# Kernel optimization log

Hardware: AMD Instinct MI355X
Metric: run time of the kernel (lower is better)

The kernel has to match this reference:

```python
import jax, jax.numpy as jnp
import numpy as np

LN_EPS = 1e-5

def layer_norm(x, g, b):
    m = x.mean(-1, keepdims=True)
    v = ((x - m) ** 2).mean(-1, keepdims=True)
    return (x - m) / jnp.sqrt(v + LN_EPS) * g + b

def gat_conv(x, src, dst, W, att_src, att_dst, bias, heads, out_ch, concat):
    # PyG GATConv (eval mode, self-loops already included in src/dst).
    N = x.shape[0]
    h = (x @ W).reshape(N, heads, out_ch)                 # [N,H,C]
    a_src = (h * att_src).sum(-1)                          # [N,H]
    a_dst = (h * att_dst).sum(-1)                          # [N,H]
    e = jax.nn.leaky_relu(a_src[src] + a_dst[dst], 0.2)   # [E,H]
    emax = jax.ops.segment_max(e, dst, num_segments=N)    # [N,H]
    ee = jnp.exp(e - emax[dst])
    denom = jax.ops.segment_sum(ee, dst, num_segments=N)  # [N,H]
    alpha = ee / (denom[dst] + 1e-16)                      # [E,H]
    out = jax.ops.segment_sum(alpha[:, :, None] * h[src], dst, num_segments=N)  # [N,H,C]
    out = out.reshape(N, heads * out_ch) if concat else out.mean(axis=1)
    return out + bias

def setup_inputs() -> dict:
    key = jax.random.key(0)
    ks = jax.random.split(key, 32)
    N, G, E = 50000, 405, 300000
    RH, GH, H = 256, 256, 4
    def w(k, shape, fan_in):
        return jax.random.normal(k, shape, dtype=jnp.float32) * (1.0 / np.sqrt(fan_in))
    d = {}
    d["x"] = jax.random.normal(ks[0], (N, G), dtype=jnp.float32)
    d["edge_index"] = jax.random.randint(ks[1], (2, E), 0, N, dtype=jnp.int64)
    # JointEncoder
    d["enc_w1"] = w(ks[2], (G, RH), G); d["enc_b1"] = jnp.zeros(RH)
    d["ln1_g"] = jnp.ones(RH); d["ln1_b"] = jnp.zeros(RH)
    d["enc_w2"] = w(ks[3], (RH, RH), RH); d["enc_b2"] = jnp.zeros(RH)
    d["ln2_g"] = jnp.ones(RH); d["ln2_b"] = jnp.zeros(RH)
    d["w1"] = w(ks[4], (RH, H * GH), RH)
    d["att_src1"] = w(ks[5], (H, GH), GH); d["att_dst1"] = w(ks[6], (H, GH), GH)
    d["bias1"] = jnp.zeros(H * GH)
    d["res1_w"] = w(ks[7], (RH, H * GH), RH); d["res1_b"] = jnp.zeros(H * GH)
    d["w2"] = w(ks[8], (H * GH, 2 * 96), H * GH)
    d["att_src2"] = w(ks[9], (2, 96), 96); d["att_dst2"] = w(ks[10], (2, 96), 96)
    d["bias2"] = jnp.zeros(2 * 96)
    d["res2_w"] = w(ks[11], (H * GH, 2 * 96), H * GH); d["res2_b"] = jnp.zeros(2 * 96)
    d["w3"] = w(ks[12], (192, 128), 192)
    d["att_src3"] = w(ks[13], (1, 128), 128); d["att_dst3"] = w(ks[14], (1, 128), 128)
    d["bias3"] = jnp.zeros(128)
    d["res3_w"] = w(ks[15], (192, 128), 192); d["res3_b"] = jnp.zeros(128)
    # MLP head
    d["mlp_w1"] = w(ks[16], (128, 64), 128); d["mlp_b1"] = jnp.zeros(64)
    d["mlp_w2"] = w(ks[17], (64, 2), 64); d["mlp_b2"] = jnp.zeros(2)
    return d

def reference(x, edge_index, enc_w1, enc_b1, ln1_g, ln1_b, enc_w2, enc_b2, ln2_g, ln2_b,
              w1, att_src1, att_dst1, bias1, res1_w, res1_b,
              w2, att_src2, att_dst2, bias2, res2_w, res2_b,
              w3, att_src3, att_dst3, bias3, res3_w, res3_b,
              mlp_w1, mlp_b1, mlp_w2, mlp_b2):
    N = x.shape[0]
    loop = jnp.arange(N, dtype=edge_index.dtype)
    src = jnp.concatenate([edge_index[0], loop])
    dst = jnp.concatenate([edge_index[1], loop])
    # JointEncoder (eval: dropout is identity)
    h = jax.nn.relu(layer_norm(x @ enc_w1 + enc_b1, ln1_g, ln1_b))
    h = jax.nn.relu(layer_norm(h @ enc_w2 + enc_b2, ln2_g, ln2_b))
    # Block 1
    idn = h
    h = jax.nn.elu(gat_conv(h, src, dst, w1, att_src1, att_dst1, bias1, 4, 256, True))
    h = h + (idn @ res1_w + res1_b)
    # Block 2
    idn = h
    h = jax.nn.elu(gat_conv(h, src, dst, w2, att_src2, att_dst2, bias2, 2, 96, True))
    h = h + (idn @ res2_w + res2_b)
    # Block 3
    idn = h
    h = jax.nn.elu(gat_conv(h, src, dst, w3, att_src3, att_dst3, bias3, 1, 128, False))
    h = h + (idn @ res3_w + res3_b)
    # MLP head
    out = jax.nn.relu(h @ mlp_w1 + mlp_b1) @ mlp_w2 + mlp_b2
    return out
```

## Files before the change

### kernel.cpp

```cpp
#include <hip/hip_runtime.h>
#include <cstddef>

#define LN_EPS 1e-5f

typedef __bf16 bf16x8 __attribute__((ext_vector_type(8)));
typedef float  f32x4  __attribute__((ext_vector_type(4)));

typedef __attribute__((address_space(3))) unsigned int lds_u32;
typedef __attribute__((address_space(1))) unsigned int glb_u32;

__device__ __forceinline__ void gl2lds16(const void* g, void* l) {
    __builtin_amdgcn_global_load_lds((const glb_u32*)g, (lds_u32*)l, 16, 0, 0);
}

__device__ __forceinline__ float b2f(ushort h) {
    return __uint_as_float(((unsigned)h) << 16);
}
__device__ __forceinline__ ushort f2b(float f) {
    unsigned u = __float_as_uint(f);
    return (ushort)((u + 0x7fffu + ((u >> 16) & 1u)) >> 16);
}
__device__ __forceinline__ unsigned pack2(float lo, float hi) {
    return (unsigned)f2b(lo) | ((unsigned)f2b(hi) << 16);
}
__device__ __forceinline__ uint2 pack4(const f32x4 v) {
    return make_uint2(pack2(v[0], v[1]), pack2(v[2], v[3]));
}

__device__ __forceinline__ void xcd_map(int& bx, int& by) {
    int NX = gridDim.x, MBr = gridDim.y;
    int L = blockIdx.y * NX + blockIdx.x;
    int G = NX * 8;
    int g = L / G;
    if (g * 8 + 8 <= MBr) {
        int r = L - g * G;
        by = g * 8 + (r & 7);
        bx = r >> 3;
    } else {
        by = L / NX;
        bx = L - by * NX;
    }
}

__device__ __forceinline__ float wave_allreduce_max(float v) {
    #pragma unroll
    for (int off = 32; off > 0; off >>= 1) v = fmaxf(v, __shfl_xor(v, off, 64));
    return v;
}
__device__ __forceinline__ float wave_allreduce_sum(float v) {
    #pragma unroll
    for (int off = 32; off > 0; off >>= 1) v += __shfl_xor(v, off, 64);
    return v;
}

__device__ __forceinline__ void stage32(const ushort* a0, const ushort* a1,
                                        const ushort* b0, const ushort* b1,
                                        ushort* __restrict__ As, ushort* __restrict__ Bs,
                                        int lb0, int lb1) {
    gl2lds16(a0, As + lb0);
    gl2lds16(a1, As + lb1);
    gl2lds16(b0, Bs + lb0);
    gl2lds16(b1, Bs + lb1);
}

__device__ __forceinline__ void mfma_loop32(const ushort* aA0, const ushort* aA1,
                                            const ushort* aB0, const ushort* aB1,
                                            ushort* __restrict__ As, ushort* __restrict__ Bs,
                                            int lb0, int lb1,
                                            int K, int wr, int wc, int cA, int l15,
                                            f32x4 acc[4][4]) {
    const int BUF = 128 * 32;
    const int nk = K >> 5;
    stage32(aA0, aA1, aB0, aB1, As, Bs, lb0, lb1);
    if (nk > 1) stage32(aA0 + 32, aA1 + 32, aB0 + 32, aB1 + 32,
                        As + BUF, Bs + BUF, lb0, lb1);
    int cur = 0;
    for (int t = 0; t < nk; t++) {
        if (t + 1 < nk) asm volatile("s_waitcnt vmcnt(4)" ::: "memory");
        else            asm volatile("s_waitcnt vmcnt(0)" ::: "memory");
        __builtin_amdgcn_s_barrier();
        __builtin_amdgcn_sched_barrier(0);
        int kn = (t + 2) * 32;
        if (kn < K) {
            int nb = cur + 2; if (nb >= 3) nb -= 3;
            stage32(aA0 + kn, aA1 + kn, aB0 + kn, aB1 + kn,
                    As + nb * BUF, Bs + nb * BUF, lb0, lb1);
        }
        const ushort* Ac = As + cur * BUF;
        const ushort* Bc = Bs + cur * BUF;
        bf16x8 af[4], bf[4];
        #pragma unroll
        for (int i = 0; i < 4; i++)
            af[i] = *reinterpret_cast<const bf16x8*>(&Ac[(wr + i * 16 + l15) * 32 + cA]);
        #pragma unroll
        for (int j = 0; j < 4; j++)
            bf[j] = *reinterpret_cast<const bf16x8*>(&Bc[(wc + j * 16 + l15) * 32 + cA]);
        #pragma unroll
        for (int i = 0; i < 4; i++)
            #pragma unroll
            for (int j = 0; j < 4; j++)
                acc[i][j] = __builtin_amdgcn_mfma_f32_16x16x32_bf16(bf[j], af[i], acc[i][j], 0, 0, 0);
        cur++; if (cur >= 3) cur -= 3;
    }
    __syncthreads();
}

template<int EPI>
__global__ __launch_bounds__(256) void bgemm(const ushort* __restrict__ A,
                                             const ushort* __restrict__ BT,
                                             const float* __restrict__ bias,
                                             void* __restrict__ out, int ldc,
                                             float* __restrict__ Rf,
                                             float* __restrict__ Sf, int Fs,
                                             int M, int Ncols, int K, int lda) {
    __shared__ ushort As[3][128 * 32];
    __shared__ ushort Bs[3][128 * 32];
    const int tid = threadIdx.x;
    int bx, by; xcd_map(bx, by);
    const int m0 = by * 128, n0 = bx * 128;
    const int w = tid >> 6, lane = tid & 63;
    const int wr = (w >> 1) * 64, wc = (w & 1) * 64;
    const int quad = lane >> 4, l15 = lane & 15;
    const int cA = (quad ^ ((l15 >> 1) & 3)) * 8;
    const int lb0 = w * 512, lb1 = lb0 + 2048;

    const int s0 = tid, s1 = tid + 256;
    const int r0 = s0 >> 2, g0 = ((s0 & 3) ^ ((s0 >> 3) & 3)) * 8;
    const int r1 = s1 >> 2, g1 = ((s1 & 3) ^ ((s1 >> 3) & 3)) * 8;
    int ga0 = m0 + r0; if (ga0 >= M) ga0 = M - 1;
    int ga1 = m0 + r1; if (ga1 >= M) ga1 = M - 1;
    const ushort* aA0 = A + (size_t)ga0 * lda + g0;
    const ushort* aA1 = A + (size_t)ga1 * lda + g1;
    const ushort* aB0 = BT + (size_t)(n0 + r0) * K + g0;
    const ushort* aB1 = BT + (size_t)(n0 + r1) * K + g1;

    f32x4 acc[4][4] = {};
    mfma_loop32(aA0, aA1, aB0, aB1, As[0], Bs[0], lb0, lb1,
                K, wr, wc, cA, l15, acc);

    if (EPI == 4) {
        if (wc == 0) {
            #pragma unroll
            for (int i = 0; i < 4; i++) {
                float o0 = 0.f, o1 = 0.f;
                #pragma unroll
                for (int j = 0; j < 4; j++) {
                    int colbase = j * 16 + quad * 4;
                    float4 bv = *reinterpret_cast<const float4*>(&bias[colbase]);
                    float bb[4] = { bv.x, bv.y, bv.z, bv.w };
                    #pragma unroll
                    for (int r = 0; r < 4; r++) {
                        float vv = fmaxf(acc[i][j][r] + bb[r], 0.f);
                        int c = colbase + r;
                        o0 += vv * Rf[2 * c];
                        o1 += vv * Rf[2 * c + 1];
                    }
                }
                o0 += __shfl_xor(o0, 16, 64); o0 += __shfl_xor(o0, 32, 64);
                o1 += __shfl_xor(o1, 16, 64); o1 += __shfl_xor(o1, 32, 64);
                int row = m0 + wr + i * 16 + l15;
                if (quad == 0 && row < M) {
                    ((float*)out)[(size_t)row * 2]     = o0 + Sf[0];
                    ((float*)out)[(size_t)row * 2 + 1] = o1 + Sf[1];
                }
            }
        }
        return;
    }

    const int twoH = Ncols - 2 * Fs;
    #pragma unroll
    for (int i = 0; i < 4; i++) {
        int row = m0 + wr + i * 16 + l15;
        if (row >= M) continue;
        #pragma unroll
        for (int j = 0; j < 4; j++) {
            int colbase = n0 + wc + j * 16 + quad * 4;
            if (EPI == 0) {
                f32x4 v = acc[i][j];
                if (bias) {
                    float4 bv = *reinterpret_cast<const float4*>(&bias[colbase]);
                    v[0] += bv.x; v[1] += bv.y; v[2] += bv.z; v[3] += bv.w;
                }
                *reinterpret_cast<f32x4*>(&((float*)out)[(size_t)row * ldc + colbase]) = v;
            } else if (EPI == 5) {
                if (colbase + 3 < Fs) {
                    *reinterpret_cast<uint2*>(&((ushort*)out)[(size_t)row * Fs + colbase]) = pack4(acc[i][j]);
                } else if (colbase >= Fs && colbase + 3 < 2 * Fs) {
                    *reinterpret_cast<f32x4*>(&Rf[(size_t)row * Fs + (colbase - Fs)]) = acc[i][j];
                } else {
                    #pragma unroll
                    for (int r = 0; r < 4; r++) {
                        int col = colbase + r;
                        if (col < 2 * Fs || col >= Ncols) continue;
                        Sf[(size_t)row * twoH + (col - 2 * Fs)] = acc[i][j][r];
                    }
                }
            }
        }
    }
}

__global__ __launch_bounds__(256) void bgemm_b1(const ushort* __restrict__ accb,
                                                const ushort* __restrict__ w1T,
                                                const ushort* __restrict__ h1b,
                                                const ushort* __restrict__ res1T,
                                                const float* __restrict__ bias1,
                                                const float* __restrict__ res1b,
                                                ushort* __restrict__ H2b, int M) {
    __shared__ ushort As[3][128 * 32];
    __shared__ ushort Bs[3][128 * 32];
    const int tid = threadIdx.x;
    int bx, by; xcd_map(bx, by);
    const int m0 = by * 128, n0 = bx * 128;
    const int h = n0 >> 8;
    const int w = tid >> 6, lane = tid & 63;
    const int wr = (w >> 1) * 64, wc = (w & 1) * 64;
    const int quad = lane >> 4, l15 = lane & 15;
    const int cA = (quad ^ ((l15 >> 1) & 3)) * 8;
    const int lb0 = w * 512, lb1 = lb0 + 2048;

    const int s0 = tid, s1 = tid + 256;
    const int r0 = s0 >> 2, g0 = ((s0 & 3) ^ ((s0 >> 3) & 3)) * 8;
    const int r1 = s1 >> 2, g1 = ((s1 & 3) ^ ((s1 >> 3) & 3)) * 8;
    int ga0 = m0 + r0; if (ga0 >= M) ga0 = M - 1;
    int ga1 = m0 + r1; if (ga1 >= M) ga1 = M - 1;

    f32x4 acc[4][4] = {};

    mfma_loop32(accb + (size_t)ga0 * 1024 + h * 256 + g0,
                accb + (size_t)ga1 * 1024 + h * 256 + g1,
                w1T + (size_t)(n0 + r0) * 256 + g0,
                w1T + (size_t)(n0 + r1) * 256 + g1,
                As[0], Bs[0], lb0, lb1, 256, wr, wc, cA, l15, acc);

    #pragma unroll
    for (int i = 0; i < 4; i++) {
        #pragma unroll
        for (int j = 0; j < 4; j++) {
            int colbase = n0 + wc + j * 16 + quad * 4;
            float4 bv = *reinterpret_cast<const float4*>(&bias1[colbase]);
            float4 rv = *reinterpret_cast<const float4*>(&res1b[colbase]);
            float bb[4] = { bv.x, bv.y, bv.z, bv.w };
            float rr[4] = { rv.x, rv.y, rv.z, rv.w };
            #pragma unroll
            for (int r = 0; r < 4; r++) {
                float t = acc[i][j][r] + bb[r];
                t = t > 0.f ? t : (__expf(t) - 1.f);
                acc[i][j][r] = t + rr[r];
            }
        }
    }

    mfma_loop32(h1b + (size_t)ga0 * 256 + g0,
                h1b + (size_t)ga1 * 256 + g1,
                res1T + (size_t)(n0 + r0) * 256 + g0,
                res1T + (size_t)(n0 + r1) * 256 + g1,
                As[0], Bs[0], lb0, lb1, 256, wr, wc, cA, l15, acc);

    #pragma unroll
    for (int i = 0; i < 4; i++) {
        int row = m0 + wr + i * 16 + l15;
        if (row >= M) continue;
        #pragma unroll
        for (int j = 0; j < 4; j++) {
            int colbase = n0 + wc + j * 16 + quad * 4;
            *reinterpret_cast<uint2*>(&H2b[(size_t)row * 1024 + colbase]) = pack4(acc[i][j]);
        }
    }
}

__global__ void conv_pad_x_kernel(const float* __restrict__ x, ushort* __restrict__ xb, int N) {
    int t = blockIdx.x * 256 + threadIdx.x;
    if (t >= N * 448) return;
    int n = t / 448, k = t - n * 448;
    xb[t] = f2b(k < 405 ? x[(size_t)n * 405 + k] : 0.f);
}

__device__ __forceinline__ void prep_seg(int t, const float* src, ushort* dst,
                                         int K, int Nreal, int Kpad, int ldsrc) {
    int n = t / Kpad, k = t - n * Kpad;
    float v = (k < K && n < Nreal) ? src[(size_t)k * ldsrc + n] : 0.f;
    dst[t] = f2b(v);
}

__global__ void prep_all_kernel(const float* __restrict__ enc_w1, const float* __restrict__ enc_w2,
                                const float* __restrict__ w1, const float* __restrict__ res1_w,
                                const float* __restrict__ w2, const float* __restrict__ res2_w,
                                const float* __restrict__ w3, const float* __restrict__ res3_w,
                                const float* __restrict__ mlp_w1,
                                ushort* __restrict__ enc_w1T, ushort* __restrict__ enc_w2T,
                                ushort* __restrict__ w1T, ushort* __restrict__ res1T,
                                ushort* __restrict__ Bcat2T, ushort* __restrict__ Bcat3T,
                                ushort* __restrict__ mlpw1T) {
    int t = blockIdx.x * 256 + threadIdx.x;
    const int c0 = 114688;
    const int c1 = c0 + 65536;
    const int c2 = c1 + 262144;
    const int c3 = c2 + 262144;
    const int c4 = c3 + 196608;
    const int c5 = c4 + 196608;
    const int c6 = c5 + 126976;
    const int c7 = c6 + 24576;
    const int c8 = c7 + 24576;
    const int c9 = c8 + 24192;
    const int c10 = c9 + 16384;
    if (t < c0)      prep_seg(t,        enc_w1, enc_w1T, 405, 256, 448, 256);
    else if (t < c1) prep_seg(t - c0,   enc_w2, enc_w2T, 256, 256, 256, 256);
    else if (t < c2) prep_seg(t - c1,   w1,     w1T,     256, 1024, 256, 1024);
    else if (t < c3) prep_seg(t - c2,   res1_w, res1T,   256, 1024, 256, 1024);
    else if (t < c4) prep_seg(t - c3,   w2,     Bcat2T,  1024, 192, 1024, 192);
    else if (t < c5) prep_seg(t - c4,   res2_w, Bcat2T + (size_t)192 * 1024, 1024, 192, 1024, 192);
    else if (t < c6) Bcat2T[(size_t)388 * 1024 + (t - c5)] = 0;
    else if (t < c7) prep_seg(t - c6,   w3,     Bcat3T,  192, 128, 192, 128);
    else if (t < c8) prep_seg(t - c7,   res3_w, Bcat3T + (size_t)128 * 192, 192, 128, 192, 128);
    else if (t < c9) Bcat3T[(size_t)258 * 192 + (t - c8)] = 0;
    else if (t < c10) prep_seg(t - c9,  mlp_w1, mlpw1T,  128, 64, 128, 64);
}

template<int H>
__global__ __launch_bounds__(256) void ln_relu_w_kernel(const float* __restrict__ x,
                                                        const float* __restrict__ g,
                                                        const float* __restrict__ b,
                                                        const float* __restrict__ qs,
                                                        const float* __restrict__ qd,
                                                        ushort* __restrict__ out,
                                                        float* __restrict__ a_s,
                                                        float* __restrict__ a_d,
                                                        int N) {
    const int lane = threadIdx.x & 63;
    int wid = blockIdx.x * 4 + (threadIdx.x >> 6);
    const int nw = gridDim.x * 4;
    const int c4 = lane * 4;

    f32x4 gv = *reinterpret_cast<const f32x4*>(&g[c4]);
    f32x4 bv = *reinterpret_cast<const f32x4*>(&b[c4]);
    f32x4 qsv[H > 0 ? H : 1], qdv[H > 0 ? H : 1];
    if (H > 0) {
        #pragma unroll
        for (int hh = 0; hh < H; hh++) {
            qsv[hh] = *reinterpret_cast<const f32x4*>(&qs[hh * 256 + c4]);
            qdv[hh] = *reinterpret_cast<const f32x4*>(&qd[hh * 256 + c4]);
        }
    }

    for (int row = wid; row < N; row += nw) {
        f32x4 v = *reinterpret_cast<const f32x4*>(&x[(size_t)row * 256 + c4]);
        float s  = v[0] + v[1] + v[2] + v[3];
        float s2 = v[0] * v[0] + v[1] * v[1] + v[2] * v[2] + v[3] * v[3];
        #pragma unroll
        for (int off = 32; off > 0; off >>= 1) {
            s  += __shfl_xor(s,  off, 64);
            s2 += __shfl_xor(s2, off, 64);
        }
        float m   = s * (1.f / 256.f);
        float var = s2 * (1.f / 256.f) - m * m;
        float rs  = rsqrtf(var + LN_EPS);
        f32x4 o;
        #pragma unroll
        for (int k = 0; k < 4; k++) o[k] = fmaxf((v[k] - m) * rs * gv[k] + bv[k], 0.f);
        *reinterpret_cast<uint2*>(&out[(size_t)row * 256 + c4]) =
            make_uint2(pack2(o[0], o[1]), pack2(o[2], o[3]));
        if (H > 0) {
            float sc[H > 0 ? 2 * H : 1];
            #pragma unroll
            for (int hh = 0; hh < H; hh++) {
                sc[hh]     = o[0] * qsv[hh][0] + o[1] * qsv[hh][1] + o[2] * qsv[hh][2] + o[3] * qsv[hh][3];
                sc[H + hh] = o[0] * qdv[hh][0] + o[1] * qdv[hh][1] + o[2] * qdv[hh][2] + o[3] * qdv[hh][3];
            }
            #pragma unroll
            for (int off = 32; off > 0; off >>= 1)
                #pragma unroll
                for (int k = 0; k < 2 * H; k++) sc[k] += __shfl_xor(sc[k], off, 64);
            if (lane == 0) {
                #pragma unroll
                for (int k = 0; k < H; k++) a_s[(size_t)row * H + k] = sc[k];
            } else if (lane == 1) {
                #pragma unroll
                for (int k = 0; k < H; k++) a_d[(size_t)row * H + k] = sc[H + k];
            }
        }
    }
}

__global__ void fold_att_kernel(const float* __restrict__ W,
                                const float* __restrict__ att_s,
                                const float* __restrict__ att_d,
                                float* __restrict__ qs, float* __restrict__ qd,
                                int Cin, int Cout, int H) {
    int t = blockIdx.x * blockDim.x + threadIdx.x;
    if (t >= H * Cin) return;
    int h = t / Cin, k = t - h * Cin;
    const float* wrow = W + (size_t)k * (H * Cout) + (size_t)h * Cout;
    const float* as = att_s + (size_t)h * Cout;
    const float* ad = att_d + (size_t)h * Cout;
    float ss = 0.f, sd = 0.f;
    for (int c = 0; c < Cout; c++) { float wv = wrow[c]; ss += wv * as[c]; sd += wv * ad[c]; }
    qs[t] = ss;
    qd[t] = sd;
}

__global__ void fold_att_b16_kernel(const float* __restrict__ W,
                                    const float* __restrict__ att_s,
                                    const float* __restrict__ att_d,
                                    ushort* __restrict__ qs_b, ushort* __restrict__ qd_b,
                                    int Cin, int Cout, int H) {
    int t = blockIdx.x * blockDim.x + threadIdx.x;
    if (t >= H * Cin) return;
    int h = t / Cin, k = t - h * Cin;
    const float* wrow = W + (size_t)k * (H * Cout) + (size_t)h * Cout;
    const float* as = att_s + (size_t)h * Cout;
    const float* ad = att_d + (size_t)h * Cout;
    float ss = 0.f, sd = 0.f;
    for (int c = 0; c < Cout; c++) { float wv = wrow[c]; ss += wv * as[c]; sd += wv * ad[c]; }
    qs_b[t] = f2b(ss);
    qd_b[t] = f2b(sd);
}

__device__ __forceinline__ void edge_sd(const int* ei, int e, int E, int& s, int& d) {
    if (e < E) { s = ei[e]; d = ei[E + e]; } else { s = d = e - E; }
}

__global__ void deg_kernel(const int* __restrict__ ei, int* __restrict__ deg, int E, int Et) {
    int e = blockIdx.x * blockDim.x + threadIdx.x;
    if (e >= Et) return;
    int s, d; edge_sd(ei, e, E, s, d);
    atomicAdd(&deg[d], 1);
}

__global__ __launch_bounds__(256) void scan1_kernel(const int* __restrict__ deg,
                                                    int* __restrict__ incl,
                                                    int* __restrict__ part, int N) {
    __shared__ int sd[256];
    int t = threadIdx.x;
    int i = blockIdx.x * 256 + t;
    int v = (i < N) ? deg[i] : 0;
    sd[t] = v; __syncthreads();
    #pragma unroll
    for (int o = 1; o < 256; o <<= 1) {
        int x = (t >= o) ? sd[t - o] : 0;
        __syncthreads();
        sd[t] += x;
        __syncthreads();
    }
    if (i < N) incl[i] = sd[t];
    if (t == 255) part[blockIdx.x] = sd[255];
}

__global__ __launch_bounds__(256) void scan2_kernel(int* __restrict__ part, int nb) {
    __shared__ int sd[256];
    int t = threadIdx.x;
    int v = (t < nb) ? part[t] : 0;
    sd[t] = v; __syncthreads();
    #pragma unroll
    for (int o = 1; o < 256; o <<= 1) {
        int x = (t >= o) ? sd[t - o] : 0;
        __syncthreads();
        sd[t] += x;
        __syncthreads();
    }
    if (t < nb) part[t] = sd[t];
}

__global__ void scan3_kernel(const int* __restrict__ incl, const int* __restrict__ deg,
                             const int* __restrict__ part, int* __restrict__ row_ptr, int N) {
    int i = blockIdx.x * blockDim.x + threadIdx.x;
    if (i >= N) return;
    int off = (blockIdx.x > 0) ? part[blockIdx.x - 1] : 0;
    row_ptr[i] = incl[i] - deg[i] + off;
}

__global__ void fill_kernel(const int* __restrict__ ei, const int* __restrict__ row_ptr,
                            int* __restrict__ cur, int* __restrict__ csr_src, int E, int Et) {
    int e = blockIdx.x * blockDim.x + threadIdx.x;
    if (e >= Et) return;
    int s, d; edge_sd(ei, e, E, s, d);
    int pos = row_ptr[d] + atomicAdd(&cur[d], 1);
    csr_src[pos] = s;
}

#define ACAP 256

__global__ __launch_bounds__(128) void aggr_b1_fused_kernel(const int* __restrict__ row_ptr,
                                                            const int* __restrict__ deg,
                                                            const int* __restrict__ csr_src,
                                                            const float* __restrict__ a_s,
                                                            const float* __restrict__ a_d,
                                                            const ushort* __restrict__ h1b,
                                                            ushort* __restrict__ accb) {
    __shared__ float alf[ACAP][4];
    __shared__ float sstat[8];
    int d = blockIdx.x, t = threadIdx.x;
    int base = row_ptr[d], dg = deg[d];
    float4 ad = *reinterpret_cast<const float4*>(&a_d[(size_t)d * 4]);
    if (t < 64) {
        float m0 = -1e30f, m1 = -1e30f, m2 = -1e30f, m3 = -1e30f;
        for (int j = t; j < dg; j += 64) {
            int s = csr_src[base + j];
            float4 sv = *reinterpret_cast<const float4*>(&a_s[(size_t)s * 4]);
            float c0 = sv.x + ad.x; c0 = c0 > 0.f ? c0 : 0.2f * c0; m0 = fmaxf(m0, c0);
            float c1 = sv.y + ad.y; c1 = c1 > 0.f ? c1 : 0.2f * c1; m1 = fmaxf(m1, c1);
            float c2 = sv.z + ad.z; c2 = c2 > 0.f ? c2 : 0.2f * c2; m2 = fmaxf(m2, c2);
            float c3 = sv.w + ad.w; c3 = c3 > 0.f ? c3 : 0.2f * c3; m3 = fmaxf(m3, c3);
        }
        m0 = wave_allreduce_max(m0); m1 = wave_allreduce_max(m1);
        m2 = wave_allreduce_max(m2); m3 = wave_allreduce_max(m3);
        float s0 = 0.f, s1 = 0.f, s2 = 0.f, s3 = 0.f;
        for (int j = t; j < dg; j += 64) {
            int s = csr_src[base + j];
            float4 sv = *reinterpret_cast<const float4*>(&a_s[(size_t)s * 4]);
            float c0 = sv.x + ad.x; c0 = c0 > 0.f ? c0 : 0.2f * c0; float e0 = __expf(c0 - m0); s0 += e0;
            float c1 = sv.y + ad.y; c1 = c1 > 0.f ? c1 : 0.2f * c1; float e1 = __expf(c1 - m1); s1 += e1;
            float c2 = sv.z + ad.z; c2 = c2 > 0.f ? c2 : 0.2f * c2; float e2 = __expf(c2 - m2); s2 += e2;
            float c3 = sv.w + ad.w; c3 = c3 > 0.f ? c3 : 0.2f * c3; float e3 = __expf(c3 - m3); s3 += e3;
            if (j < ACAP) { alf[j][0] = e0; alf[j][1] = e1; alf[j][2] = e2; alf[j][3] = e3; }
        }
        s0 = wave_allreduce_sum(s0); s1 = wave_allreduce_sum(s1);
        s2 = wave_allreduce_sum(s2); s3 = wave_allreduce_sum(s3);
        if (t == 0) {
            sstat[0] = m0; sstat[1] = m1; sstat[2] = m2; sstat[3] = m3;
            sstat[4] = 1.f / (s0 + 1e-16f); sstat[5] = 1.f / (s1 + 1e-16f);
            sstat[6] = 1.f / (s2 + 1e-16f); sstat[7] = 1.f / (s3 + 1e-16f);
        }
    }
    __syncthreads();
    float r0 = sstat[4], r1 = sstat[5], r2 = sstat[6], r3 = sstat[7];
    float a00 = 0, a01 = 0, a10 = 0, a11 = 0, a20 = 0, a21 = 0, a30 = 0, a31 = 0;
    for (int j = 0; j < dg; j++) {
        int s = csr_src[base + j];
        float al0, al1, al2, al3;
        if (j < ACAP) {
            al0 = alf[j][0] * r0; al1 = alf[j][1] * r1;
            al2 = alf[j][2] * r2; al3 = alf[j][3] * r3;
        } else {
            float4 sv = *reinterpret_cast<const float4*>(&a_s[(size_t)s * 4]);
            float c0 = sv.x + ad.x; c0 = c0 > 0.f ? c0 : 0.2f * c0; al0 = __expf(c0 - sstat[0]) * r0;
            float c1 = sv.y + ad.y; c1 = c1 > 0.f ? c1 : 0.2f * c1; al1 = __expf(c1 - sstat[1]) * r1;
            float c2 = sv.z + ad.z; c2 = c2 > 0.f ? c2 : 0.2f * c2; al2 = __expf(c2 - sstat[2]) * r2;
            float c3 = sv.w + ad.w; c3 = c3 > 0.f ? c3 : 0.2f * c3; al3 = __expf(c3 - sstat[3]) * r3;
        }
        unsigned v = reinterpret_cast<const unsigned*>(h1b + (size_t)s * 256)[t];
        float lo = b2f((ushort)(v & 0xffff)), hi = b2f((ushort)(v >> 16));
        a00 += al0 * lo; a01 += al0 * hi;
        a10 += al1 * lo; a11 += al1 * hi;
        a20 += al2 * lo; a21 += al2 * hi;
        a30 += al3 * lo; a31 += al3 * hi;
    }
    unsigned* o = reinterpret_cast<unsigned*>(accb + (size_t)d * 1024);
    o[t]       = pack2(a00, a01);
    o[t + 128] = pack2(a10, a11);
    o[t + 256] = pack2(a20, a21);
    o[t + 384] = pack2(a30, a31);
}

template<int H, int C, int F, int NT>
__global__ __launch_bounds__(NT) void aggr_comb_fused_kernel(const int* __restrict__ row_ptr,
                                                             const int* __restrict__ deg,
                                                             const int* __restrict__ csr_src,
                                                             const float* __restrict__ as,
                                                             const ushort* __restrict__ g,
                                                             const float* __restrict__ Rf,
                                                             const float* __restrict__ gb,
                                                             const float* __restrict__ rb,
                                                             ushort* __restrict__ outb) {
    __shared__ float alf[ACAP][H];
    __shared__ float sstat[2 * H];
    int d = blockIdx.x;
    int t = threadIdx.x;
    int base = row_ptr[d], dg = deg[d];
    if (t < 64) {
        float ad[H], mx[H];
        #pragma unroll
        for (int h = 0; h < H; h++) { ad[h] = as[(size_t)d * 2 * H + H + h]; mx[h] = -1e30f; }
        for (int j = t; j < dg; j += 64) {
            int s = csr_src[base + j];
            #pragma unroll
            for (int h = 0; h < H; h++) {
                float c = as[(size_t)s * 2 * H + h] + ad[h];
                c = c > 0.f ? c : 0.2f * c;
                mx[h] = fmaxf(mx[h], c);
            }
        }
        #pragma unroll
        for (int h = 0; h < H; h++) mx[h] = wave_allreduce_max(mx[h]);
        float sm[H];
        #pragma unroll
        for (int h = 0; h < H; h++) sm[h] = 0.f;
        for (int j = t; j < dg; j += 64) {
            int s = csr_src[base + j];
            #pragma unroll
            for (int h = 0; h < H; h++) {
                float c = as[(size_t)s * 2 * H + h] + ad[h];
                c = c > 0.f ? c : 0.2f * c;
                float e = __expf(c - mx[h]);
                sm[h] += e;
                if (j < ACAP) alf[j][h] = e;
            }
        }
        #pragma unroll
        for (int h = 0; h < H; h++) sm[h] = wave_allreduce_sum(sm[h]);
        if (t == 0) {
            #pragma unroll
            for (int h = 0; h < H; h++) { sstat[h] = mx[h]; sstat[H + h] = 1.f / (sm[h] + 1e-16f); }
        }
    }
    __syncthreads();
    int hd = (2 * t) / C;
    float mxv = sstat[hd], rdv = sstat[H + hd];
    float adv = as[(size_t)d * 2 * H + H + hd];
    float lo = 0.f, hi = 0.f;
    for (int j = 0; j < dg; j++) {
        int s = csr_src[base + j];
        float al;
        if (j < ACAP) al = alf[j][hd] * rdv;
        else {
            float c = as[(size_t)s * 2 * H + hd] + adv;
            c = c > 0.f ? c : 0.2f * c;
            al = __expf(c - mxv) * rdv;
        }
        unsigned v = reinterpret_cast<const unsigned*>(g + (size_t)s * F)[t];
        lo += al * b2f((ushort)(v & 0xffff));
        hi += al * b2f((ushort)(v >> 16));
    }
    int c0 = 2 * t, c1 = 2 * t + 1;
    float o0 = lo + gb[c0]; o0 = o0 > 0.f ? o0 : (__expf(o0) - 1.f);
    float o1 = hi + gb[c1]; o1 = o1 > 0.f ? o1 : (__expf(o1) - 1.f);
    o0 += Rf[(size_t)d * F + c0] + rb[c0];
    o1 += Rf[(size_t)d * F + c1] + rb[c1];
    reinterpret_cast<unsigned*>(outb)[(size_t)d * (F / 2) + t] = pack2(o0, o1);
}

extern "C" void kernel_launch(void* const* d_in, const int* in_sizes, int n_in,
                              void* d_out, int out_size, void* d_ws, size_t ws_size,
                              hipStream_t stream) {
    const float* x        = (const float*)d_in[0];
    const int*   ei       = (const int*)d_in[1];
    const float* enc_w1   = (const float*)d_in[2];
    const float* enc_b1   = (const float*)d_in[3];
    const float* ln1_g    = (const float*)d_in[4];
    const float* ln1_b    = (const float*)d_in[5];
    const float* enc_w2   = (const float*)d_in[6];
    const float* enc_b2   = (const float*)d_in[7];
    const float* ln2_g    = (const float*)d_in[8];
    const float* ln2_b    = (const float*)d_in[9];
    const float* w1       = (const float*)d_in[10];
    const float* att_src1 = (const float*)d_in[11];
    const float* att_dst1 = (const float*)d_in[12];
    const float* bias1    = (const float*)d_in[13];
    const float* res1_w   = (const float*)d_in[14];
    const float* res1_b   = (const float*)d_in[15];
    const float* w2       = (const float*)d_in[16];
    const float* att_src2 = (const float*)d_in[17];
    const float* att_dst2 = (const float*)d_in[18];
    const float* bias2    = (const float*)d_in[19];
    const float* res2_w   = (const float*)d_in[20];
    const float* res2_b   = (const float*)d_in[21];
    const float* w3       = (const float*)d_in[22];
    const float* att_src3 = (const float*)d_in[23];
    const float* att_dst3 = (const float*)d_in[24];
    const float* bias3    = (const float*)d_in[25];
    const float* res3_w   = (const float*)d_in[26];
    const float* res3_b   = (const float*)d_in[27];
    const float* mlp_w1   = (const float*)d_in[28];
    const float* mlp_b1   = (const float*)d_in[29];
    const float* mlp_w2   = (const float*)d_in[30];
    const float* mlp_b2   = (const float*)d_in[31];

    const int N  = in_sizes[0] / 405;
    const int E  = in_sizes[1] / 2;
    const int Et = E + N;
    const int NB = (N + 255) / 256;

    char* p = (char*)d_ws;
    char* R0 = p;
    char* R1 = R0 + (size_t)N * 896;
    char* R2 = R1 + (size_t)N * 512;
    char* R3 = R2 + (size_t)N * 512;
    char* R4 = R3 + (size_t)N * 2048;
    char* T  = R4 + (size_t)N * 2048;

    ushort* xb   = (ushort*)R0;
    ushort* H3b  = (ushort*)R0;
    ushort* h0b  = (ushort*)R1;
    ushort* G2b  = (ushort*)R1;
    ushort* h1b  = (ushort*)R2;
    ushort* G3b  = (ushort*)R2;
    ushort* H4b  = (ushort*)(R2 + (size_t)N * 256);
    float*  F1   = (float*)R3;
    ushort* H2b  = (ushort*)R3;
    ushort* accb = (ushort*)R4;
    float*  Rf   = (float*)R4;

    float* a_s   = (float*)T;                         T += (size_t)N * 4 * 4;
    float* a_d   = (float*)T;                         T += (size_t)N * 4 * 4;
    float* qs    = (float*)T;                         T += 2048 * 4;
    float* qd    = (float*)T;                         T += 2048 * 4;
    int* deg     = (int*)T;                           T += (size_t)N * 4;
    int* cur     = (int*)T;                           T += (size_t)N * 4;
    int* row_ptr = (int*)T;                           T += (size_t)N * 4;
    int* incl    = (int*)T;                           T += (size_t)N * 4;
    int* part    = (int*)T;                           T += 256 * 4;
    int* csr_src = (int*)T;                           T += (size_t)Et * 4;
    ushort* enc_w1T = (ushort*)T;                     T += (size_t)256 * 448 * 2;
    ushort* enc_w2T = (ushort*)T;                     T += (size_t)256 * 256 * 2;
    ushort* w1T     = (ushort*)T;                     T += (size_t)1024 * 256 * 2;
    ushort* res1T   = (ushort*)T;                     T += (size_t)1024 * 256 * 2;
    ushort* Bcat2T  = (ushort*)T;                     T += (size_t)512 * 1024 * 2;
    ushort* Bcat3T  = (ushort*)T;                     T += (size_t)384 * 192 * 2;
    ushort* mlpw1T  = (ushort*)T;                     T += (size_t)128 * 128 * 2;

    auto cdiv = [](int a, int b) { return (a + b - 1) / b; };
    const int MB = cdiv(N, 128);

    hipMemsetAsync(deg, 0, (size_t)N * 8, stream);
    deg_kernel<<<cdiv(Et, 256), 256, 0, stream>>>(ei, deg, E, Et);
    scan1_kernel<<<NB, 256, 0, stream>>>(deg, incl, part, N);
    scan2_kernel<<<1, 256, 0, stream>>>(part, NB);
    scan3_kernel<<<NB, 256, 0, stream>>>(incl, deg, part, row_ptr, N);
    fill_kernel<<<cdiv(Et, 256), 256, 0, stream>>>(ei, row_ptr, cur, csr_src, E, Et);

    prep_all_kernel<<<cdiv(1314432, 256), 256, 0, stream>>>(
        enc_w1, enc_w2, w1, res1_w, w2, res2_w, w3, res3_w, mlp_w1,
        enc_w1T, enc_w2T, w1T, res1T, Bcat2T, Bcat3T, mlpw1T);

    fold_att_kernel<<<cdiv(4 * 256, 256), 256, 0, stream>>>(w1, att_src1, att_dst1, qs, qd, 256, 256, 4);

    conv_pad_x_kernel<<<cdiv(N * 448, 256), 256, 0, stream>>>(x, xb, N);
    bgemm<0><<<dim3(2, MB), 256, 0, stream>>>(xb, enc_w1T, enc_b1, F1, 256, nullptr, nullptr, 0, N, 256, 448, 448);
    ln_relu_w_kernel<0><<<1024, 256, 0, stream>>>(F1, ln1_g, ln1_b, nullptr, nullptr, h0b, nullptr, nullptr, N);
    bgemm<0><<<dim3(2, MB), 256, 0, stream>>>(h0b, enc_w2T, enc_b2, F1, 256, nullptr, nullptr, 0, N, 256, 256, 256);
    ln_relu_w_kernel<4><<<1024, 256, 0, stream>>>(F1, ln2_g, ln2_b, qs, qd, h1b, a_s, a_d, N);

    aggr_b1_fused_kernel<<<N, 128, 0, stream>>>(row_ptr, deg, csr_src, a_s, a_d, h1b, accb);
    bgemm_b1<<<dim3(8, MB), 256, 0, stream>>>(accb, w1T, h1b, res1T, bias1, res1_b, H2b, N);

    {
        fold_att_b16_kernel<<<cdiv(2 * 1024, 256), 256, 0, stream>>>(w2, att_src2, att_dst2,
            Bcat2T + (size_t)384 * 1024, Bcat2T + (size_t)386 * 1024, 1024, 96, 2);
        bgemm<5><<<dim3(4, MB), 256, 0, stream>>>(H2b, Bcat2T, nullptr, G2b, 0, Rf, a_s, 192, N, 388, 1024, 1024);
        aggr_comb_fused_kernel<2, 96, 192, 96><<<N, 96, 0, stream>>>(row_ptr, deg, csr_src, a_s,
                                                                     G2b, Rf, bias2, res2_b, H3b);
    }

    {
        fold_att_b16_kernel<<<1, 256, 0, stream>>>(w3, att_src3, att_dst3,
            Bcat3T + (size_t)256 * 192, Bcat3T + (size_t)257 * 192, 192, 128, 1);
        bgemm<5><<<dim3(3, MB), 256, 0, stream>>>(H3b, Bcat3T, nullptr, G3b, 0, Rf, a_s, 128, N, 258, 192, 192);
        aggr_comb_fused_kernel<1, 128, 128, 64><<<N, 64, 0, stream>>>(row_ptr, deg, csr_src, a_s,
                                                                      G3b, Rf, bias3, res3_b, H4b);
    }

    bgemm<4><<<dim3(1, MB), 256, 0, stream>>>(H4b, mlpw1T, mlp_b1, d_out, 2,
                                              (float*)mlp_w2, (float*)mlp_b2, 0, N, 64, 128, 128);
}
```

Baseline: 809.1 us.

## Enlarge GEMM tiles to 256x128 with 512-thread blocks and double buffering

All bf16 GEMM kernels now use 8 waves per block and a 256-row M tile, so each staged B tile is shared by twice as many rows. The three-stage LDS pipeline becomes a two-stage double buffer that waits for all loads each step. The aim is better B reuse and fewer blocks, with bounds set for higher occupancy. The cost is less latency hiding from the shallower pipeline, and tail blocks may be less balanced at N=50000.

```diff
diff --git a/kernel.cpp b/kernel.cpp
--- a/kernel.cpp
+++ b/kernel.cpp
@@ -53,41 +53,34 @@
     return v;
 }
 
-__device__ __forceinline__ void stage32(const ushort* a0, const ushort* a1,
-                                        const ushort* b0, const ushort* b1,
-                                        ushort* __restrict__ As, ushort* __restrict__ Bs,
-                                        int lb0, int lb1) {
-    gl2lds16(a0, As + lb0);
-    gl2lds16(a1, As + lb1);
-    gl2lds16(b0, Bs + lb0);
-    gl2lds16(b1, Bs + lb1);
-}
-
-__device__ __forceinline__ void mfma_loop32(const ushort* aA0, const ushort* aA1,
-                                            const ushort* aB0, const ushort* aB1,
-                                            ushort* __restrict__ As, ushort* __restrict__ Bs,
-                                            int lb0, int lb1,
-                                            int K, int wr, int wc, int cA, int l15,
-                                            f32x4 acc[4][4]) {
-    const int BUF = 128 * 32;
+__device__ __forceinline__ void stage3(const ushort* a0, const ushort* a1, const ushort* b0,
+                                       ushort* __restrict__ As, ushort* __restrict__ Bs,
+                                       int lb) {
+    gl2lds16(a0, As + lb);
+    gl2lds16(a1, As + lb + 4096);
+    gl2lds16(b0, Bs + lb);
+}
+
+__device__ __forceinline__ void mfma_loop256(const ushort* aA0, const ushort* aA1,
+                                             const ushort* aB0,
+                                             ushort* __restrict__ As, ushort* __restrict__ Bs,
+                                             int lb,
+                                             int K, int wr, int wc, int cA, int l15,
+                                             f32x4 acc[4][4]) {
+    const int BUFA = 256 * 32;
+    const int BUFB = 128 * 32;
     const int nk = K >> 5;
-    stage32(aA0, aA1, aB0, aB1, As, Bs, lb0, lb1);
-    if (nk > 1) stage32(aA0 + 32, aA1 + 32, aB0 + 32, aB1 + 32,
-                        As + BUF, Bs + BUF, lb0, lb1);
-    int cur = 0;
+    stage3(aA0, aA1, aB0, As, Bs, lb);
+    int p = 0;
     for (int t = 0; t < nk; t++) {
-        if (t + 1 < nk) asm volatile("s_waitcnt vmcnt(4)" ::: "memory");
-        else            asm volatile("s_waitcnt vmcnt(0)" ::: "memory");
+        asm volatile("s_waitcnt vmcnt(0)" ::: "memory");
         __builtin_amdgcn_s_barrier();
         __builtin_amdgcn_sched_barrier(0);
-        int kn = (t + 2) * 32;
-        if (kn < K) {
-            int nb = cur + 2; if (nb >= 3) nb -= 3;
-            stage32(aA0 + kn, aA1 + kn, aB0 + kn, aB1 + kn,
-                    As + nb * BUF, Bs + nb * BUF, lb0, lb1);
-        }
-        const ushort* Ac = As + cur * BUF;
-        const ushort* Bc = Bs + cur * BUF;
+        int kn = (t + 1) * 32;
+        if (kn < K) stage3(aA0 + kn, aA1 + kn, aB0 + kn,
+                           As + (p ^ 1) * BUFA, Bs + (p ^ 1) * BUFB, lb);
+        const ushort* Ac = As + p * BUFA;
+        const ushort* Bc = Bs + p * BUFB;
         bf16x8 af[4], bf[4];
         #pragma unroll
         for (int i = 0; i < 4; i++)
@@ -100,43 +93,39 @@
             #pragma unroll
             for (int j = 0; j < 4; j++)
                 acc[i][j] = __builtin_amdgcn_mfma_f32_16x16x32_bf16(bf[j], af[i], acc[i][j], 0, 0, 0);
-        cur++; if (cur >= 3) cur -= 3;
+        p ^= 1;
     }
     __syncthreads();
 }
 
 template<int EPI>
-__global__ __launch_bounds__(256) void bgemm(const ushort* __restrict__ A,
-                                             const ushort* __restrict__ BT,
-                                             const float* __restrict__ bias,
-                                             void* __restrict__ out, int ldc,
-                                             float* __restrict__ Rf,
-                                             float* __restrict__ Sf, int Fs,
-                                             int M, int Ncols, int K, int lda) {
-    __shared__ ushort As[3][128 * 32];
-    __shared__ ushort Bs[3][128 * 32];
+__global__ __launch_bounds__(512, 4) void bgemm(const ushort* __restrict__ A,
+                                                const ushort* __restrict__ BT,
+                                                const float* __restrict__ bias,
+                                                void* __restrict__ out, int ldc,
+                                                float* __restrict__ Rf,
+                                                float* __restrict__ Sf, int Fs,
+                                                int M, int Ncols, int K, int lda) {
+    __shared__ ushort As[2][256 * 32];
+    __shared__ ushort Bs[2][128 * 32];
     const int tid = threadIdx.x;
     int bx, by; xcd_map(bx, by);
-    const int m0 = by * 128, n0 = bx * 128;
+    const int m0 = by * 256, n0 = bx * 128;
     const int w = tid >> 6, lane = tid & 63;
     const int wr = (w >> 1) * 64, wc = (w & 1) * 64;
     const int quad = lane >> 4, l15 = lane & 15;
     const int cA = (quad ^ ((l15 >> 1) & 3)) * 8;
-    const int lb0 = w * 512, lb1 = lb0 + 2048;
-
-    const int s0 = tid, s1 = tid + 256;
-    const int r0 = s0 >> 2, g0 = ((s0 & 3) ^ ((s0 >> 3) & 3)) * 8;
-    const int r1 = s1 >> 2, g1 = ((s1 & 3) ^ ((s1 >> 3) & 3)) * 8;
-    int ga0 = m0 + r0; if (ga0 >= M) ga0 = M - 1;
-    int ga1 = m0 + r1; if (ga1 >= M) ga1 = M - 1;
-    const ushort* aA0 = A + (size_t)ga0 * lda + g0;
-    const ushort* aA1 = A + (size_t)ga1 * lda + g1;
-    const ushort* aB0 = BT + (size_t)(n0 + r0) * K + g0;
-    const ushort* aB1 = BT + (size_t)(n0 + r1) * K + g1;
+    const int lb = w * 512;
+
+    const int r = tid >> 2, g = ((tid & 3) ^ ((tid >> 3) & 3)) * 8;
+    int ga0 = m0 + r;       if (ga0 >= M) ga0 = M - 1;
+    int ga1 = m0 + 128 + r; if (ga1 >= M) ga1 = M - 1;
+    const ushort* aA0 = A + (size_t)ga0 * lda + g;
+    const ushort* aA1 = A + (size_t)ga1 * lda + g;
+    const ushort* aB0 = BT + (size_t)(n0 + r) * K + g;
 
     f32x4 acc[4][4] = {};
-    mfma_loop32(aA0, aA1, aB0, aB1, As[0], Bs[0], lb0, lb1,
-                K, wr, wc, cA, l15, acc);
+    mfma_loop256(aA0, aA1, aB0, As[0], Bs[0], lb, K, wr, wc, cA, l15, acc);
 
     if (EPI == 4) {
         if (wc == 0) {
@@ -149,9 +138,9 @@
                     float4 bv = *reinterpret_cast<const float4*>(&bias[colbase]);
                     float bb[4] = { bv.x, bv.y, bv.z, bv.w };
                     #pragma unroll
-                    for (int r = 0; r < 4; r++) {
-                        float vv = fmaxf(acc[i][j][r] + bb[r], 0.f);
-                        int c = colbase + r;
+                    for (int rr = 0; rr < 4; rr++) {
+                        float vv = fmaxf(acc[i][j][rr] + bb[rr], 0.f);
+                        int c = colbase + rr;
                         o0 += vv * Rf[2 * c];
                         o1 += vv * Rf[2 * c + 1];
                     }
@@ -190,10 +179,10 @@
                     *reinterpret_cast<f32x4*>(&Rf[(size_t)row * Fs + (colbase - Fs)]) = acc[i][j];
                 } else {
                     #pragma unroll
-                    for (int r = 0; r < 4; r++) {
-                        int col = colbase + r;
+                    for (int rr = 0; rr < 4; rr++) {
+                        int col = colbase + rr;
                         if (col < 2 * Fs || col >= Ncols) continue;
-                        Sf[(size_t)row * twoH + (col - 2 * Fs)] = acc[i][j][r];
+                        Sf[(size_t)row * twoH + (col - 2 * Fs)] = acc[i][j][rr];
                     }
                 }
             }
@@ -201,38 +190,35 @@
     }
 }
 
-__global__ __launch_bounds__(256) void bgemm_b1(const ushort* __restrict__ accb,
-                                                const ushort* __restrict__ w1T,
-                                                const ushort* __restrict__ h1b,
-                                                const ushort* __restrict__ res1T,
-                                                const float* __restrict__ bias1,
-                                                const float* __restrict__ res1b,
-                                                ushort* __restrict__ H2b, int M) {
-    __shared__ ushort As[3][128 * 32];
-    __shared__ ushort Bs[3][128 * 32];
+__global__ __launch_bounds__(512, 4) void bgemm_b1(const ushort* __restrict__ accb,
+                                                   const ushort* __restrict__ w1T,
+                                                   const ushort* __restrict__ h1b,
+                                                   const ushort* __restrict__ res1T,
+                                                   const float* __restrict__ bias1,
+                                                   const float* __restrict__ res1b,
+                                                   ushort* __restrict__ H2b, int M) {
+    __shared__ ushort As[2][256 * 32];
+    __shared__ ushort Bs[2][128 * 32];
     const int tid = threadIdx.x;
     int bx, by; xcd_map(bx, by);
-    const int m0 = by * 128, n0 = bx * 128;
+    const int m0 = by * 256, n0 = bx * 128;
     const int h = n0 >> 8;
     const int w = tid >> 6, lane = tid & 63;
     const int wr = (w >> 1) * 64, wc = (w & 1) * 64;
     const int quad = lane >> 4, l15 = lane & 15;
     const int cA = (quad ^ ((l15 >> 1) & 3)) * 8;
-    const int lb0 = w * 512, lb1 = lb0 + 2048;
-
-    const int s0 = tid, s1 = tid + 256;
-    const int r0 = s0 >> 2, g0 = ((s0 & 3) ^ ((s0 >> 3) & 3)) * 8;
-    const int r1 = s1 >> 2, g1 = ((s1 & 3) ^ ((s1 >> 3) & 3)) * 8;
-    int ga0 = m0 + r0; if (ga0 >= M) ga0 = M - 1;
-    int ga1 = m0 + r1; if (ga1 >= M) ga1 = M - 1;
+    const int lb = w * 512;
+
+    const int r = tid >> 2, g = ((tid & 3) ^ ((tid >> 3) & 3)) * 8;
+    int ga0 = m0 + r;       if (ga0 >= M) ga0 = M - 1;
+    int ga1 = m0 + 128 + r; if (ga1 >= M) ga1 = M - 1;
 
     f32x4 acc[4][4] = {};
 
-    mfma_loop32(accb + (size_t)ga0 * 1024 + h * 256 + g0,
-                accb + (size_t)ga1 * 1024 + h * 256 + g1,
-                w1T + (size_t)(n0 + r0) * 256 + g0,
-                w1T + (size_t)(n0 + r1) * 256 + g1,
-                As[0], Bs[0], lb0, lb1, 256, wr, wc, cA, l15, acc);
+    mfma_loop256(accb + (size_t)ga0 * 1024 + h * 256 + g,
+                 accb + (size_t)ga1 * 1024 + h * 256 + g,
+                 w1T + (size_t)(n0 + r) * 256 + g,
+                 As[0], Bs[0], lb, 256, wr, wc, cA, l15, acc);
 
     #pragma unroll
     for (int i = 0; i < 4; i++) {
@@ -244,19 +230,18 @@
             float bb[4] = { bv.x, bv.y, bv.z, bv.w };
             float rr[4] = { rv.x, rv.y, rv.z, rv.w };
             #pragma unroll
-            for (int r = 0; r < 4; r++) {
-                float t = acc[i][j][r] + bb[r];
+            for (int q = 0; q < 4; q++) {
+                float t = acc[i][j][q] + bb[q];
                 t = t > 0.f ? t : (__expf(t) - 1.f);
-                acc[i][j][r] = t + rr[r];
+                acc[i][j][q] = t + rr[q];
             }
         }
     }
 
-    mfma_loop32(h1b + (size_t)ga0 * 256 + g0,
-                h1b + (size_t)ga1 * 256 + g1,
-                res1T + (size_t)(n0 + r0) * 256 + g0,
-                res1T + (size_t)(n0 + r1) * 256 + g1,
-                As[0], Bs[0], lb0, lb1, 256, wr, wc, cA, l15, acc);
+    mfma_loop256(h1b + (size_t)ga0 * 256 + g,
+                 h1b + (size_t)ga1 * 256 + g,
+                 res1T + (size_t)(n0 + r) * 256 + g,
+                 As[0], Bs[0], lb, 256, wr, wc, cA, l15, acc);
 
     #pragma unroll
     for (int i = 0; i < 4; i++) {
@@ -653,8 +638,8 @@
     const float* att_src2 = (const float*)d_in[17];
     const float* att_dst2 = (const float*)d_in[18];
     const float* bias2    = (const float*)d_in[19];
+    const float* res2_b_  = (const float*)d_in[21];
     const float* res2_w   = (const float*)d_in[20];
-    const float* res2_b   = (const float*)d_in[21];
     const float* w3       = (const float*)d_in[22];
     const float* att_src3 = (const float*)d_in[23];
     const float* att_dst3 = (const float*)d_in[24];
@@ -665,6 +650,7 @@
     const float* mlp_b1   = (const float*)d_in[29];
     const float* mlp_w2   = (const float*)d_in[30];
     const float* mlp_b2   = (const float*)d_in[31];
+    const float* res2_b   = res2_b_;
 
     const int N  = in_sizes[0] / 405;
     const int E  = in_sizes[1] / 2;
@@ -710,7 +696,7 @@
     ushort* mlpw1T  = (ushort*)T;                     T += (size_t)128 * 128 * 2;
 
     auto cdiv = [](int a, int b) { return (a + b - 1) / b; };
-    const int MB = cdiv(N, 128);
+    const int MBr = cdiv(N, 256);
 
     hipMemsetAsync(deg, 0, (size_t)N * 8, stream);
     deg_kernel<<<cdiv(Et, 256), 256, 0, stream>>>(ei, deg, E, Et);
@@ -726,18 +712,18 @@
     fold_att_kernel<<<cdiv(4 * 256, 256), 256, 0, stream>>>(w1, att_src1, att_dst1, qs, qd, 256, 256, 4);
 
     conv_pad_x_kernel<<<cdiv(N * 448, 256), 256, 0, stream>>>(x, xb, N);
-    bgemm<0><<<dim3(2, MB), 256, 0, stream>>>(xb, enc_w1T, enc_b1, F1, 256, nullptr, nullptr, 0, N, 256, 448, 448);
+    bgemm<0><<<dim3(2, MBr), 512, 0, stream>>>(xb, enc_w1T, enc_b1, F1, 256, nullptr, nullptr, 0, N, 256, 448, 448);
     ln_relu_w_kernel<0><<<1024, 256, 0, stream>>>(F1, ln1_g, ln1_b, nullptr, nullptr, h0b, nullptr, nullptr, N);
-    bgemm<0><<<dim3(2, MB), 256, 0, stream>>>(h0b, enc_w2T, enc_b2, F1, 256, nullptr, nullptr, 0, N, 256, 256, 256);
+    bgemm<0><<<dim3(2, MBr), 512, 0, stream>>>(h0b, enc_w2T, enc_b2, F1, 256, nullptr, nullptr, 0, N, 256, 256, 256);
     ln_relu_w_kernel<4><<<1024, 256, 0, stream>>>(F1, ln2_g, ln2_b, qs, qd, h1b, a_s, a_d, N);
 
     aggr_b1_fused_kernel<<<N, 128, 0, stream>>>(row_ptr, deg, csr_src, a_s, a_d, h1b, accb);
-    bgemm_b1<<<dim3(8, MB), 256, 0, stream>>>(accb, w1T, h1b, res1T, bias1, res1_b, H2b, N);
+    bgemm_b1<<<dim3(8, MBr), 512, 0, stream>>>(accb, w1T, h1b, res1T, bias1, res1_b, H2b, N);
 
     {
         fold_att_b16_kernel<<<cdiv(2 * 1024, 256), 256, 0, stream>>>(w2, att_src2, att_dst2,
             Bcat2T + (size_t)384 * 1024, Bcat2T + (size_t)386 * 1024, 1024, 96, 2);
-        bgemm<5><<<dim3(4, MB), 256, 0, stream>>>(H2b, Bcat2T, nullptr, G2b, 0, Rf, a_s, 192, N, 388, 1024, 1024);
+        bgemm<5><<<dim3(4, MBr), 512, 0, stream>>>(H2b, Bcat2T, nullptr, G2b, 0, Rf, a_s, 192, N, 388, 1024, 1024);
         aggr_comb_fused_kernel<2, 96, 192, 96><<<N, 96, 0, stream>>>(row_ptr, deg, csr_src, a_s,
                                                                      G2b, Rf, bias2, res2_b, H3b);
     }
@@ -745,11 +731,11 @@
     {
         fold_att_b16_kernel<<<1, 256, 0, stream>>>(w3, att_src3, att_dst3,
             Bcat3T + (size_t)256 * 192, Bcat3T + (size_t)257 * 192, 192, 128, 1);
-        bgemm<5><<<dim3(3, MB), 256, 0, stream>>>(H3b, Bcat3T, nullptr, G3b, 0, Rf, a_s, 128, N, 258, 192, 192);
+        bgemm<5><<<dim3(3, MBr), 512, 0, stream>>>(H3b, Bcat3T, nullptr, G3b, 0, Rf, a_s, 128, N, 258, 192, 192);
         aggr_comb_fused_kernel<1, 128, 128, 64><<<N, 64, 0, stream>>>(row_ptr, deg, csr_src, a_s,
                                                                       G3b, Rf, bias3, res3_b, H4b);
     }
 
-    bgemm<4><<<dim3(1, MB), 256, 0, stream>>>(H4b, mlpw1T, mlp_b1, d_out, 2,
-                                              (float*)mlp_w2, (float*)mlp_b2, 0, N, 64, 128, 128);
-}
+    bgemm<4><<<dim3(1, MBr), 512, 0, stream>>>(H4b, mlpw1T, mlp_b1, d_out, 2,
+                                               (float*)mlp_w2, (float*)mlp_b2, 0, N, 64, 128, 128);
+}
```

Result: no change. 803.1 us (-0.7%).
